# Performance work log

Hardware: AMD Instinct MI355X
Metric: run time of the kernel (lower is better)

Reference implementation:

```python
import jax, jax.numpy as jnp
import numpy as np

N_NODES = 50000
N_EDGES = 800000
HIDDEN = 128
N_GRAPHS = 32
EPS = 1e-5  # GraphNorm eps


def setup_inputs() -> dict:
    key = jax.random.key(0)
    ks = jax.random.split(key, 8)
    x = jax.random.normal(ks[0], (N_NODES, HIDDEN), dtype=jnp.float32)
    edge_index = jax.random.randint(ks[1], (2, N_EDGES), 0, N_NODES, dtype=jnp.int64)
    batch = jnp.sort(jax.random.randint(ks[2], (N_NODES,), 0, N_GRAPHS, dtype=jnp.int64))
    s = 1.0 / np.sqrt(HIDDEN)
    # SAGEConv: lin_l (applied to aggregated neighbors, with bias) and lin_r (root, no bias)
    W_l = jax.random.normal(ks[3], (HIDDEN, HIDDEN), dtype=jnp.float32) * s
    b_l = jnp.zeros((HIDDEN,), dtype=jnp.float32)
    W_r = jax.random.normal(ks[4], (HIDDEN, HIDDEN), dtype=jnp.float32) * s
    # GraphNorm params: weight, bias, mean_scale (alpha)
    gn_weight = jnp.ones((HIDDEN,), dtype=jnp.float32)
    gn_bias = jnp.zeros((HIDDEN,), dtype=jnp.float32)
    gn_mean_scale = jnp.ones((HIDDEN,), dtype=jnp.float32)
    return {
        "x": x, "edge_index": edge_index, "batch": batch,
        "W_l": W_l, "b_l": b_l, "W_r": W_r,
        "gn_weight": gn_weight, "gn_bias": gn_bias, "gn_mean_scale": gn_mean_scale,
    }


def reference(x, edge_index, batch, W_l, b_l, W_r, gn_weight, gn_bias, gn_mean_scale):
    src, dst = edge_index[0], edge_index[1]
    n = x.shape[0]
    # --- SAGEConv: mean aggregation of source features at destination ---
    msg_sum = jax.ops.segment_sum(x[src], dst, num_segments=n)          # [N, D]
    deg = jax.ops.segment_sum(jnp.ones((src.shape[0],), x.dtype), dst, num_segments=n)
    agg = msg_sum / jnp.maximum(deg, 1.0)[:, None]
    out = agg @ W_l + b_l + x @ W_r                                      # [N, D]
    # --- GraphNorm: per-graph mean/var with learnable mean scale alpha ---
    g_cnt = jax.ops.segment_sum(jnp.ones((n,), x.dtype), batch, num_segments=N_GRAPHS)[:, None]
    g_cnt = jnp.maximum(g_cnt, 1.0)
    mean = jax.ops.segment_sum(out, batch, num_segments=N_GRAPHS) / g_cnt  # [G, D]
    sub = out - gn_mean_scale * mean[batch]
    var = jax.ops.segment_sum(sub * sub, batch, num_segments=N_GRAPHS) / g_cnt
    normed = gn_weight * sub / jnp.sqrt(var[batch] + EPS) + gn_bias
    # --- exact GELU (torch nn.GELU default), dropout = identity (eval), residual ---
    return jax.nn.gelu(normed, approximate=False) + x
```

## Files before the change

kernel.cpp:

```cpp
#include <hip/hip_runtime.h>
#include <math.h>

#define NN 50000
#define NE 800000
#define HD 128
#define NG 32
#define GN_EPS 1e-5f
#define NSH 8

#define NBLK_R 800
#define CH_R   1000
#define NBUCK  196
#define NBB    (NBUCK * NBLK_R)
#define NCHS   ((NBB + 255) / 256)
#define DCAP   8192

typedef __bf16 v8bf __attribute__((ext_vector_type(8)));
typedef float f32x4 __attribute__((ext_vector_type(4)));

#define ROWPTR_OFF 0
#define BB_OFF     50016
#define CS_OFF     206816
#define GSUMS_OFF  207840
#define GSQS_OFF   240608
#define GCNTS_OFF  273376
#define MEAN_OFF   273632
#define RSTD_OFF   277728
#define SRCS_OFF   281824
#define PSRC_OFF   681824
#define PDLOW_OFF  1081824
#define WPACK_OFF  1281824
#define MEMSET_INTS (32768 + 32768 + 256)

__device__ __forceinline__ unsigned short f2bf(float f) {
  unsigned int u = __float_as_uint(f);
  u = (u + 0x7fffu + ((u >> 16) & 1u)) >> 16;
  return (unsigned short)u;
}
__device__ __forceinline__ float bf_lo(unsigned int u) { return __uint_as_float(u << 16); }
__device__ __forceinline__ float bf_hi(unsigned int u) { return __uint_as_float(u & 0xffff0000u); }

__global__ __launch_bounds__(256) void prep_k(const float* __restrict__ x,
    const float* __restrict__ Wl, const float* __restrict__ Wr,
    unsigned short* __restrict__ Abuf, unsigned short* __restrict__ wp,
    int* __restrict__ zbase) {
  int i = blockIdx.x * 256 + threadIdx.x;
  if (i < MEMSET_INTS) zbase[i] = 0;
  if (i < 32768) {
    int e = i & 7, lane = (i >> 3) & 63, nt = (i >> 9) & 7, ks = i >> 12;
    int k = ks * 32 + (lane >> 4) * 8 + e;
    int c = nt * 16 + (lane & 15);
    float v = (k < HD) ? Wl[k * HD + c] : Wr[(k - HD) * HD + c];
    wp[i] = f2bf(v);
  }
  if (i < NN * 16) {
    int n = i >> 4, seg = i & 15;
    const float* src = x + (size_t)n * HD + seg * 8;
    float4 v0 = *(const float4*)(src);
    float4 v1 = *(const float4*)(src + 4);
    uint4 o;
    o.x = (unsigned)f2bf(v0.x) | ((unsigned)f2bf(v0.y) << 16);
    o.y = (unsigned)f2bf(v0.z) | ((unsigned)f2bf(v0.w) << 16);
    o.z = (unsigned)f2bf(v1.x) | ((unsigned)f2bf(v1.y) << 16);
    o.w = (unsigned)f2bf(v1.z) | ((unsigned)f2bf(v1.w) << 16);
    *(uint4*)(Abuf + (size_t)n * 256 + 128 + seg * 8) = o;
  }
}


__global__ __launch_bounds__(256) void rhist_k(const int* __restrict__ ei,
                                               int* __restrict__ bb) {
  __shared__ int h[NBUCK];
  int tid = threadIdx.x, b = blockIdx.x;
  for (int i = tid; i < NBUCK; i += 256) h[i] = 0;
  __syncthreads();
  int base = b * CH_R;
  for (int j = tid; j < CH_R; j += 256)
    atomicAdd(&h[ei[NE + base + j] >> 8], 1);
  __syncthreads();
  for (int i = tid; i < NBUCK; i += 256) bb[i * NBLK_R + b] = h[i];
}

__global__ __launch_bounds__(256) void csum_k(const int* __restrict__ bb,
                                              int* __restrict__ cs) {
  __shared__ int red[4];
  int i = blockIdx.x * 256 + threadIdx.x;
  int v = (i < NBB) ? bb[i] : 0;
#pragma unroll
  for (int off = 32; off; off >>= 1) v += __shfl_down(v, off, 64);
  if ((threadIdx.x & 63) == 0) red[threadIdx.x >> 6] = v;
  __syncthreads();
  if (threadIdx.x == 0) cs[blockIdx.x] = red[0] + red[1] + red[2] + red[3];
}

__global__ __launch_bounds__(1024) void cscan_k(int* __restrict__ cs) {
  __shared__ int s[1024];
  int t = threadIdx.x;
  int v = (t < NCHS) ? cs[t] : 0;
  s[t] = v;
  __syncthreads();
  for (int off = 1; off < 1024; off <<= 1) {
    int u = (t >= off) ? s[t - off] : 0;
    __syncthreads();
    s[t] += u;
    __syncthreads();
  }
  if (t < NCHS) cs[t] = s[t] - v;
}

__global__ __launch_bounds__(256) void cfill_k(int* __restrict__ bb,
                                               const int* __restrict__ cs) {
  __shared__ int s[256];
  int t = threadIdx.x;
  int i = blockIdx.x * 256 + t;
  int c = (i < NBB) ? bb[i] : 0;
  s[t] = c;
  __syncthreads();
#pragma unroll
  for (int off = 1; off < 256; off <<= 1) {
    int u = (t >= off) ? s[t - off] : 0;
    __syncthreads();
    s[t] += u;
    __syncthreads();
  }
  if (i < NBB) bb[i] = cs[blockIdx.x] + s[t] - c;
}

__global__ __launch_bounds__(256) void rscatter_k(const int* __restrict__ ei,
    const int* __restrict__ bb, unsigned short* __restrict__ psrc,
    unsigned char* __restrict__ pdlow) {
  __shared__ int cur[NBUCK];
  int tid = threadIdx.x, b = blockIdx.x;
  for (int i = tid; i < NBUCK; i += 256) cur[i] = bb[i * NBLK_R + b];
  __syncthreads();
  int base = b * CH_R;
  for (int j = tid; j < CH_R; j += 256) {
    int e = base + j;
    int src = ei[e];
    int dst = ei[NE + e];
    int pos = atomicAdd(&cur[dst >> 8], 1);
    psrc[pos] = (unsigned short)src;
    pdlow[pos] = (unsigned char)(dst & 255);
  }
}

__global__ __launch_bounds__(256) void rfinal_k(const int* __restrict__ bb,
    const unsigned short* __restrict__ psrc, const unsigned char* __restrict__ pdlow,
    unsigned short* __restrict__ srcs, int* __restrict__ rowptr) {
  __shared__ unsigned short ssrc[DCAP];
  __shared__ unsigned short sout[DCAP];
  __shared__ unsigned char sdl[DCAP];
  __shared__ int h2[256], scn[256], cur2[256];
  int tid = threadIdx.x, k = blockIdx.x;
  int segB = bb[k * NBLK_R];
  int segE = (k == NBUCK - 1) ? NE : bb[(k + 1) * NBLK_R];
  int cnt = segE - segB;
  for (int j = tid; j < cnt; j += 256) {
    ssrc[j] = psrc[segB + j];
    sdl[j] = pdlow[segB + j];
  }
  h2[tid] = 0;
  __syncthreads();
  for (int j = tid; j < cnt; j += 256) atomicAdd(&h2[sdl[j]], 1);
  __syncthreads();
  scn[tid] = h2[tid];
  __syncthreads();
#pragma unroll
  for (int off = 1; off < 256; off <<= 1) {
    int u = (tid >= off) ? scn[tid - off] : 0;
    __syncthreads();
    scn[tid] += u;
    __syncthreads();
  }
  int excl = scn[tid] - h2[tid];
  cur2[tid] = excl;
  int dst = k * 256 + tid;
  if (dst < NN) rowptr[dst] = segB + excl;
  if (dst == NN - 1) rowptr[NN] = NE;
  __syncthreads();
  for (int j = tid; j < cnt; j += 256) {
    int p = atomicAdd(&cur2[sdl[j]], 1);
    sout[p] = ssrc[j];
  }
  __syncthreads();
  for (int j = tid; j < cnt; j += 256) srcs[segB + j] = sout[j];
}

__global__ __launch_bounds__(256) void gather_k(const int* __restrict__ rowptr,
    const unsigned short* __restrict__ srcs, unsigned short* Abuf) {
  int t = blockIdx.x * 256 + threadIdx.x;
  int n = t >> 4, q = t & 15;
  if (n >= NN) return;
  int b = rowptr[n], e = rowptr[n + 1];
  float a0=0,a1=0,a2=0,a3=0,a4=0,a5=0,a6=0,a7=0;
  int i = b;
  for (; i + 1 < e; i += 2) {
    int s0 = srcs[i], s1 = srcs[i + 1];
    uint4 v0 = *(const uint4*)(Abuf + (size_t)s0 * 256 + 128 + q * 8);
    uint4 v1 = *(const uint4*)(Abuf + (size_t)s1 * 256 + 128 + q * 8);
    a0 += bf_lo(v0.x) + bf_lo(v1.x);  a1 += bf_hi(v0.x) + bf_hi(v1.x);
    a2 += bf_lo(v0.y) + bf_lo(v1.y);  a3 += bf_hi(v0.y) + bf_hi(v1.y);
    a4 += bf_lo(v0.z) + bf_lo(v1.z);  a5 += bf_hi(v0.z) + bf_hi(v1.z);
    a6 += bf_lo(v0.w) + bf_lo(v1.w);  a7 += bf_hi(v0.w) + bf_hi(v1.w);
  }
  if (i < e) {
    int s0 = srcs[i];
    uint4 v0 = *(const uint4*)(Abuf + (size_t)s0 * 256 + 128 + q * 8);
    a0 += bf_lo(v0.x); a1 += bf_hi(v0.x);
    a2 += bf_lo(v0.y); a3 += bf_hi(v0.y);
    a4 += bf_lo(v0.z); a5 += bf_hi(v0.z);
    a6 += bf_lo(v0.w); a7 += bf_hi(v0.w);
  }
  float inv = 1.0f / fmaxf((float)(e - b), 1.0f);
  uint4 o;
  o.x = (unsigned)f2bf(a0 * inv) | ((unsigned)f2bf(a1 * inv) << 16);
  o.y = (unsigned)f2bf(a2 * inv) | ((unsigned)f2bf(a3 * inv) << 16);
  o.z = (unsigned)f2bf(a4 * inv) | ((unsigned)f2bf(a5 * inv) << 16);
  o.w = (unsigned)f2bf(a6 * inv) | ((unsigned)f2bf(a7 * inv) << 16);
  *(uint4*)(Abuf + (size_t)n * 256 + q * 8) = o;
}

__global__ __launch_bounds__(256) void gemm_k(const unsigned short* Abuf,
    const unsigned short* __restrict__ wp, const float* __restrict__ bl,
    const int* __restrict__ batch, float* out, float* __restrict__ gsumS,
    float* __restrict__ gsqS, float* __restrict__ gcntS) {
  __shared__ float lsum[16][136];
  __shared__ float lsq[16][136];
  __shared__ unsigned char ridx[64];
  __shared__ int sg0, snrun;
  int tid = threadIdx.x;
  int base0 = blockIdx.x * 64;
  int nvalid = min(64, NN - base0);
  if (tid == 0) {
    int g0 = batch[base0];
    sg0 = g0;
    snrun = batch[base0 + nvalid - 1] - g0 + 1;
  }
  __syncthreads();
  if (tid < 64)
    ridx[tid] = (tid < nvalid) ? (unsigned char)(batch[base0 + tid] - sg0)
                               : (unsigned char)0;
  __syncthreads();

  int shard = blockIdx.x & 7;
  float* gs = gsumS + shard * (NG * HD);
  float* gq = gsqS + shard * (NG * HD);
  float* gc = gcntS + shard * NG;

  int wave = tid >> 6;
  int lane = tid & 63;
  int base = base0 + wave * 16;
  int row = lane & 15, kg = lane >> 4;
  int node = base + row;
  if (node > NN - 1) node = NN - 1;
  const unsigned short* arow = Abuf + (size_t)node * 256 + kg * 8;
  f32x4 acc[8] = {};
#pragma unroll
  for (int ks = 0; ks < 8; ++ks) {
    v8bf a = __builtin_bit_cast(v8bf, *(const uint4*)(arow + ks * 32));
    const unsigned short* wrow = wp + ks * 4096 + lane * 8;
#pragma unroll
    for (int nt = 0; nt < 8; ++nt) {
      v8bf b = __builtin_bit_cast(v8bf, *(const uint4*)(wrow + nt * 512));
      acc[nt] = __builtin_amdgcn_mfma_f32_16x16x32_bf16(a, b, acc[nt], 0, 0, 0);
    }
  }
  int c0 = lane & 15;
  float bv[8];
#pragma unroll
  for (int nt = 0; nt < 8; ++nt) bv[nt] = bl[nt * 16 + c0];

  if (snrun == 1) {
    float ps0[8] = {}, pq0[8] = {};
#pragma unroll
    for (int j = 0; j < 4; ++j) {
      int n = base0 + wave * 16 + kg * 4 + j;
      if (n >= NN) break;
      float* orow = out + (size_t)n * HD;
#pragma unroll
      for (int nt = 0; nt < 8; ++nt) {
        float v = acc[nt][j] + bv[nt];
        orow[nt * 16 + c0] = v;
        ps0[nt] += v;
        pq0[nt] += v * v;
      }
    }
    int r = wave * 4 + kg;
#pragma unroll
    for (int nt = 0; nt < 8; ++nt) {
      lsum[r][nt * 16 + c0] = ps0[nt];
      lsq[r][nt * 16 + c0] = pq0[nt];
    }
    __syncthreads();
    if (tid < HD) {
      float s = 0.0f, q = 0.0f;
#pragma unroll
      for (int r2 = 0; r2 < 16; ++r2) { s += lsum[r2][tid]; q += lsq[r2][tid]; }
      atomicAdd(gs + sg0 * HD + tid, s);
      atomicAdd(gq + sg0 * HD + tid, q);
    }
    if (tid == 0) atomicAdd(gc + sg0, (float)nvalid);
  } else if (snrun == 2) {
    float ps0[8] = {}, pq0[8] = {}, ps1[8] = {}, pq1[8] = {};
#pragma unroll
    for (int j = 0; j < 4; ++j) {
      int rb = wave * 16 + kg * 4 + j;
      int n = base0 + rb;
      if (n >= NN) break;
      float* orow = out + (size_t)n * HD;
      bool b1 = (ridx[rb] != 0);
#pragma unroll
      for (int nt = 0; nt < 8; ++nt) {
        float v = acc[nt][j] + bv[nt];
        orow[nt * 16 + c0] = v;
        if (b1) { ps1[nt] += v; pq1[nt] += v * v; }
        else    { ps0[nt] += v; pq0[nt] += v * v; }
      }
    }
    int r = wave * 4 + kg;
#pragma unroll
    for (int nt = 0; nt < 8; ++nt) {
      lsum[r][nt * 16 + c0] = ps0[nt];
      lsq[r][nt * 16 + c0] = pq0[nt];
    }
    __syncthreads();
    if (tid < HD) {
      float s = 0.0f, q = 0.0f;
#pragma unroll
      for (int r2 = 0; r2 < 16; ++r2) { s += lsum[r2][tid]; q += lsq[r2][tid]; }
      atomicAdd(gs + sg0 * HD + tid, s);
      atomicAdd(gq + sg0 * HD + tid, q);
    }
    __syncthreads();
#pragma unroll
    for (int nt = 0; nt < 8; ++nt) {
      lsum[r][nt * 16 + c0] = ps1[nt];
      lsq[r][nt * 16 + c0] = pq1[nt];
    }
    __syncthreads();
    if (tid < HD) {
      float s = 0.0f, q = 0.0f;
#pragma unroll
      for (int r2 = 0; r2 < 16; ++r2) { s += lsum[r2][tid]; q += lsq[r2][tid]; }
      atomicAdd(gs + (sg0 + 1) * HD + tid, s);
      atomicAdd(gq + (sg0 + 1) * HD + tid, q);
    }
    if (tid == 0) {
      int n0 = 0;
      for (int r2 = 0; r2 < nvalid; ++r2) n0 += (ridx[r2] == 0);
      atomicAdd(gc + sg0, (float)n0);
      atomicAdd(gc + sg0 + 1, (float)(nvalid - n0));
    }
  } else {
#pragma unroll
    for (int j = 0; j < 4; ++j) {
      int rb = wave * 16 + kg * 4 + j;
      int n = base0 + rb;
      if (n >= NN) break;
      float* orow = out + (size_t)n * HD;
      int g = sg0 + ridx[rb];
#pragma unroll
      for (int nt = 0; nt < 8; ++nt) {
        float v = acc[nt][j] + bv[nt];
        orow[nt * 16 + c0] = v;
        atomicAdd(gs + g * HD + nt * 16 + c0, v);
        atomicAdd(gq + g * HD + nt * 16 + c0, v * v);
      }
    }
    if (tid < nvalid) atomicAdd(gc + batch[base0 + tid], 1.0f);
  }
}

__global__ __launch_bounds__(256) void finalize_k(const float* __restrict__ gsumS,
    const float* __restrict__ gsqS, const float* __restrict__ gcntS,
    const float* __restrict__ alpha, float* __restrict__ mean,
    float* __restrict__ rstd) {
  int i = blockIdx.x * 256 + threadIdx.x;
  if (i >= NG * HD) return;
  int g = i >> 7, d = i & 127;
  float s = 0.0f, q = 0.0f, cnt = 0.0f;
#pragma unroll
  for (int sh = 0; sh < NSH; ++sh) {
    s += gsumS[sh * (NG * HD) + i];
    q += gsqS[sh * (NG * HD) + i];
    cnt += gcntS[sh * NG + g];
  }
  cnt = fmaxf(cnt, 1.0f);
  float mu = s / cnt;
  float a = alpha[d];
  float var = q / cnt - mu * mu * (2.0f * a - a * a);
  mean[i] = mu;
  rstd[i] = rsqrtf(fmaxf(var, 0.0f) + GN_EPS);
}

__global__ __launch_bounds__(256) void final_k(float* __restrict__ out,
    const float* __restrict__ x, const int* __restrict__ batch,
    const float* __restrict__ mean, const float* __restrict__ rstd,
    const float* __restrict__ alpha, const float* __restrict__ gw,
    const float* __restrict__ gb) {
  size_t i = ((size_t)blockIdx.x * 256 + threadIdx.x) * 4;
  if (i >= (size_t)NN * HD) return;
  int n = (int)(i >> 7);
  int d = (int)(i & 127);
  int g = batch[n];
  float4 v  = *(float4*)(out + i);
  float4 xv = *(const float4*)(x + i);
  float4 al = *(const float4*)(alpha + d);
  float4 w  = *(const float4*)(gw + d);
  float4 b  = *(const float4*)(gb + d);
  float4 mn = *(const float4*)(mean + (size_t)g * HD + d);
  float4 rs = *(const float4*)(rstd + (size_t)g * HD + d);
  float vv[4] = {v.x, v.y, v.z, v.w};
  float xx[4] = {xv.x, xv.y, xv.z, xv.w};
  float aa[4] = {al.x, al.y, al.z, al.w};
  float ww[4] = {w.x, w.y, w.z, w.w};
  float bb2[4] = {b.x, b.y, b.z, b.w};
  float mm[4] = {mn.x, mn.y, mn.z, mn.w};
  float rr[4] = {rs.x, rs.y, rs.z, rs.w};
  float r[4];
#pragma unroll
  for (int c = 0; c < 4; ++c) {
    float sub = vv[c] - aa[c] * mm[c];
    float nm  = ww[c] * sub * rr[c] + bb2[c];
    float ge  = 0.5f * nm * (1.0f + erff(nm * 0.70710678118654752f));
    r[c] = ge + xx[c];
  }
  float4 res = {r[0], r[1], r[2], r[3]};
  *(float4*)(out + i) = res;
}

extern "C" void kernel_launch(void* const* d_in, const int* in_sizes, int n_in,
                              void* d_out, int out_size, void* d_ws, size_t ws_size,
                              hipStream_t stream) {
  const float* x     = (const float*)d_in[0];
  const int*   ei    = (const int*)d_in[1];
  const int*   batch = (const int*)d_in[2];
  const float* Wl    = (const float*)d_in[3];
  const float* bl    = (const float*)d_in[4];
  const float* Wr    = (const float*)d_in[5];
  const float* gw    = (const float*)d_in[6];
  const float* gb    = (const float*)d_in[7];
  const float* alpha = (const float*)d_in[8];

  float* out = (float*)d_out;
  unsigned short* Abuf = (unsigned short*)d_out;
  int*   wsi = (int*)d_ws;
  float* wsf = (float*)d_ws;
  int* rowptr = wsi + ROWPTR_OFF;
  int* bb     = wsi + BB_OFF;
  int* cs     = wsi + CS_OFF;
  float* gsumS = wsf + GSUMS_OFF;
  float* gsqS  = wsf + GSQS_OFF;
  float* gcntS = wsf + GCNTS_OFF;
  float* mean  = wsf + MEAN_OFF;
  float* rstd  = wsf + RSTD_OFF;
  unsigned short* srcs  = (unsigned short*)(wsi + SRCS_OFF);
  unsigned short* psrc  = (unsigned short*)(wsi + PSRC_OFF);
  unsigned char*  pdlow = (unsigned char*)(wsi + PDLOW_OFF);
  unsigned short* wpack = (unsigned short*)(wsi + WPACK_OFF);

  prep_k<<<3125, 256, 0, stream>>>(x, Wl, Wr, Abuf, wpack,
                                   (int*)(wsf + GSUMS_OFF));

  rhist_k<<<NBLK_R, 256, 0, stream>>>(ei, bb);
  csum_k<<<NCHS, 256, 0, stream>>>(bb, cs);
  cscan_k<<<1, 1024, 0, stream>>>(cs);
  cfill_k<<<NCHS, 256, 0, stream>>>(bb, cs);
  rscatter_k<<<NBLK_R, 256, 0, stream>>>(ei, bb, psrc, pdlow);
  rfinal_k<<<NBUCK, 256, 0, stream>>>(bb, psrc, pdlow, srcs, rowptr);

  gather_k<<<(NN * 16 + 255) / 256, 256, 0, stream>>>(rowptr, srcs, Abuf);

  gemm_k<<<(NN + 63) / 64, 256, 0, stream>>>(Abuf, wpack, bl, batch, out,
                                             gsumS, gsqS, gcntS);

  finalize_k<<<16, 256, 0, stream>>>(gsumS, gsqS, gcntS, alpha, mean, rstd);

  final_k<<<(NN * HD / 4 + 255) / 256, 256, 0, stream>>>(
      out, x, batch, mean, rstd, alpha, gw, gb);
}
```

Baseline: 106.1 us.

## Fuse neighbor gather into GEMM via LDS and merge prep with histogram

The mean-aggregation gather is moved into the GEMM kernel: each block computes the aggregated bf16 rows for its 64 nodes into shared memory and reads the root features from a separate compact bf16 buffer in the workspace. This removes one kernel launch and the global write and re-read of the aggregated half of the A buffer. The prep and destination-histogram kernels are merged into a single launch split by block index, and the histogram and scatter kernels now load edges as int4 vectors. The cost is extra LDS use and per-block gather latency ahead of the MFMA work, which may lower occupancy in the GEMM kernel.

```diff
diff --git a/kernel.cpp b/kernel.cpp
--- a/kernel.cpp
+++ b/kernel.cpp
@@ -14,6 +14,7 @@
 #define NBB    (NBUCK * NBLK_R)
 #define NCHS   ((NBB + 255) / 256)
 #define DCAP   8192
+#define PREP_BLKS 3125
 
 typedef __bf16 v8bf __attribute__((ext_vector_type(8)));
 typedef float f32x4 __attribute__((ext_vector_type(4)));
@@ -30,6 +31,7 @@
 #define PSRC_OFF   681824
 #define PDLOW_OFF  1081824
 #define WPACK_OFF  1281824
+#define ABX_OFF    1298208
 #define MEMSET_INTS (32768 + 32768 + 256)
 
 __device__ __forceinline__ unsigned short f2bf(float f) {
@@ -40,45 +42,49 @@
 __device__ __forceinline__ float bf_lo(unsigned int u) { return __uint_as_float(u << 16); }
 __device__ __forceinline__ float bf_hi(unsigned int u) { return __uint_as_float(u & 0xffff0000u); }
 
-__global__ __launch_bounds__(256) void prep_k(const float* __restrict__ x,
+__global__ __launch_bounds__(256) void prep_rhist_k(const float* __restrict__ x,
     const float* __restrict__ Wl, const float* __restrict__ Wr,
-    unsigned short* __restrict__ Abuf, unsigned short* __restrict__ wp,
-    int* __restrict__ zbase) {
-  int i = blockIdx.x * 256 + threadIdx.x;
-  if (i < MEMSET_INTS) zbase[i] = 0;
-  if (i < 32768) {
-    int e = i & 7, lane = (i >> 3) & 63, nt = (i >> 9) & 7, ks = i >> 12;
-    int k = ks * 32 + (lane >> 4) * 8 + e;
-    int c = nt * 16 + (lane & 15);
-    float v = (k < HD) ? Wl[k * HD + c] : Wr[(k - HD) * HD + c];
-    wp[i] = f2bf(v);
-  }
-  if (i < NN * 16) {
-    int n = i >> 4, seg = i & 15;
-    const float* src = x + (size_t)n * HD + seg * 8;
-    float4 v0 = *(const float4*)(src);
-    float4 v1 = *(const float4*)(src + 4);
-    uint4 o;
-    o.x = (unsigned)f2bf(v0.x) | ((unsigned)f2bf(v0.y) << 16);
-    o.y = (unsigned)f2bf(v0.z) | ((unsigned)f2bf(v0.w) << 16);
-    o.z = (unsigned)f2bf(v1.x) | ((unsigned)f2bf(v1.y) << 16);
-    o.w = (unsigned)f2bf(v1.z) | ((unsigned)f2bf(v1.w) << 16);
-    *(uint4*)(Abuf + (size_t)n * 256 + 128 + seg * 8) = o;
-  }
-}
-
-
-__global__ __launch_bounds__(256) void rhist_k(const int* __restrict__ ei,
-                                               int* __restrict__ bb) {
+    unsigned short* __restrict__ Abx, unsigned short* __restrict__ wp,
+    int* __restrict__ zbase, const int* __restrict__ ei, int* __restrict__ bb) {
   __shared__ int h[NBUCK];
-  int tid = threadIdx.x, b = blockIdx.x;
-  for (int i = tid; i < NBUCK; i += 256) h[i] = 0;
-  __syncthreads();
-  int base = b * CH_R;
-  for (int j = tid; j < CH_R; j += 256)
-    atomicAdd(&h[ei[NE + base + j] >> 8], 1);
-  __syncthreads();
-  for (int i = tid; i < NBUCK; i += 256) bb[i * NBLK_R + b] = h[i];
+  int tid = threadIdx.x;
+  if (blockIdx.x < PREP_BLKS) {
+    int i = blockIdx.x * 256 + tid;
+    if (i < MEMSET_INTS) zbase[i] = 0;
+    if (i < 32768) {
+      int e = i & 7, lane = (i >> 3) & 63, nt = (i >> 9) & 7, ks = i >> 12;
+      int k = ks * 32 + (lane >> 4) * 8 + e;
+      int c = nt * 16 + (lane & 15);
+      float v = (k < HD) ? Wl[k * HD + c] : Wr[(k - HD) * HD + c];
+      wp[i] = f2bf(v);
+    }
+    if (i < NN * 16) {
+      int n = i >> 4, seg = i & 15;
+      const float* src = x + (size_t)n * HD + seg * 8;
+      float4 v0 = *(const float4*)(src);
+      float4 v1 = *(const float4*)(src + 4);
+      uint4 o;
+      o.x = (unsigned)f2bf(v0.x) | ((unsigned)f2bf(v0.y) << 16);
+      o.y = (unsigned)f2bf(v0.z) | ((unsigned)f2bf(v0.w) << 16);
+      o.z = (unsigned)f2bf(v1.x) | ((unsigned)f2bf(v1.y) << 16);
+      o.w = (unsigned)f2bf(v1.z) | ((unsigned)f2bf(v1.w) << 16);
+      *(uint4*)(Abx + (size_t)n * HD + seg * 8) = o;
+    }
+  } else {
+    int b = blockIdx.x - PREP_BLKS;
+    for (int i = tid; i < NBUCK; i += 256) h[i] = 0;
+    __syncthreads();
+    int base = b * CH_R;
+    if (tid < CH_R / 4) {
+      int4 d = *(const int4*)(ei + NE + base + tid * 4);
+      atomicAdd(&h[d.x >> 8], 1);
+      atomicAdd(&h[d.y >> 8], 1);
+      atomicAdd(&h[d.z >> 8], 1);
+      atomicAdd(&h[d.w >> 8], 1);
+    }
+    __syncthreads();
+    for (int i = tid; i < NBUCK; i += 256) bb[i * NBLK_R + b] = h[i];
+  }
 }
 
 __global__ __launch_bounds__(256) void csum_k(const int* __restrict__ bb,
@@ -134,13 +140,14 @@
   for (int i = tid; i < NBUCK; i += 256) cur[i] = bb[i * NBLK_R + b];
   __syncthreads();
   int base = b * CH_R;
-  for (int j = tid; j < CH_R; j += 256) {
-    int e = base + j;
-    int src = ei[e];
-    int dst = ei[NE + e];
-    int pos = atomicAdd(&cur[dst >> 8], 1);
-    psrc[pos] = (unsigned short)src;
-    pdlow[pos] = (unsigned char)(dst & 255);
+  if (tid < CH_R / 4) {
+    int4 s4 = *(const int4*)(ei + base + tid * 4);
+    int4 d4 = *(const int4*)(ei + NE + base + tid * 4);
+    int p;
+    p = atomicAdd(&cur[d4.x >> 8], 1); psrc[p] = (unsigned short)s4.x; pdlow[p] = (unsigned char)(d4.x & 255);
+    p = atomicAdd(&cur[d4.y >> 8], 1); psrc[p] = (unsigned short)s4.y; pdlow[p] = (unsigned char)(d4.y & 255);
+    p = atomicAdd(&cur[d4.z >> 8], 1); psrc[p] = (unsigned short)s4.z; pdlow[p] = (unsigned char)(d4.z & 255);
+    p = atomicAdd(&cur[d4.w >> 8], 1); psrc[p] = (unsigned short)s4.w; pdlow[p] = (unsigned char)(d4.w & 255);
   }
 }
 
@@ -186,44 +193,13 @@
   for (int j = tid; j < cnt; j += 256) srcs[segB + j] = sout[j];
 }
 
-__global__ __launch_bounds__(256) void gather_k(const int* __restrict__ rowptr,
-    const unsigned short* __restrict__ srcs, unsigned short* Abuf) {
-  int t = blockIdx.x * 256 + threadIdx.x;
-  int n = t >> 4, q = t & 15;
-  if (n >= NN) return;
-  int b = rowptr[n], e = rowptr[n + 1];
-  float a0=0,a1=0,a2=0,a3=0,a4=0,a5=0,a6=0,a7=0;
-  int i = b;
-  for (; i + 1 < e; i += 2) {
-    int s0 = srcs[i], s1 = srcs[i + 1];
-    uint4 v0 = *(const uint4*)(Abuf + (size_t)s0 * 256 + 128 + q * 8);
-    uint4 v1 = *(const uint4*)(Abuf + (size_t)s1 * 256 + 128 + q * 8);
-    a0 += bf_lo(v0.x) + bf_lo(v1.x);  a1 += bf_hi(v0.x) + bf_hi(v1.x);
-    a2 += bf_lo(v0.y) + bf_lo(v1.y);  a3 += bf_hi(v0.y) + bf_hi(v1.y);
-    a4 += bf_lo(v0.z) + bf_lo(v1.z);  a5 += bf_hi(v0.z) + bf_hi(v1.z);
-    a6 += bf_lo(v0.w) + bf_lo(v1.w);  a7 += bf_hi(v0.w) + bf_hi(v1.w);
-  }
-  if (i < e) {
-    int s0 = srcs[i];
-    uint4 v0 = *(const uint4*)(Abuf + (size_t)s0 * 256 + 128 + q * 8);
-    a0 += bf_lo(v0.x); a1 += bf_hi(v0.x);
-    a2 += bf_lo(v0.y); a3 += bf_hi(v0.y);
-    a4 += bf_lo(v0.z); a5 += bf_hi(v0.z);
-    a6 += bf_lo(v0.w); a7 += bf_hi(v0.w);
-  }
-  float inv = 1.0f / fmaxf((float)(e - b), 1.0f);
-  uint4 o;
-  o.x = (unsigned)f2bf(a0 * inv) | ((unsigned)f2bf(a1 * inv) << 16);
-  o.y = (unsigned)f2bf(a2 * inv) | ((unsigned)f2bf(a3 * inv) << 16);
-  o.z = (unsigned)f2bf(a4 * inv) | ((unsigned)f2bf(a5 * inv) << 16);
-  o.w = (unsigned)f2bf(a6 * inv) | ((unsigned)f2bf(a7 * inv) << 16);
-  *(uint4*)(Abuf + (size_t)n * 256 + q * 8) = o;
-}
-
-__global__ __launch_bounds__(256) void gemm_k(const unsigned short* Abuf,
+__global__ __launch_bounds__(256) void gemm_k(const unsigned short* __restrict__ Abx,
+    const int* __restrict__ rowptr, const unsigned short* __restrict__ srcs,
     const unsigned short* __restrict__ wp, const float* __restrict__ bl,
-    const int* __restrict__ batch, float* out, float* __restrict__ gsumS,
-    float* __restrict__ gsqS, float* __restrict__ gcntS) {
+    const int* __restrict__ batch, float* __restrict__ out,
+    float* __restrict__ gsumS, float* __restrict__ gsqS,
+    float* __restrict__ gcntS) {
+  __shared__ unsigned short agg[64][136];
   __shared__ float lsum[16][136];
   __shared__ float lsq[16][136];
   __shared__ unsigned char ridx[64];
@@ -236,10 +212,46 @@
     sg0 = g0;
     snrun = batch[base0 + nvalid - 1] - g0 + 1;
   }
-  __syncthreads();
-  if (tid < 64)
-    ridx[tid] = (tid < nvalid) ? (unsigned char)(batch[base0 + tid] - sg0)
+  if (tid < 64) {
+    int nb = base0 + tid;
+    ridx[tid] = (tid < nvalid) ? (unsigned char)(batch[nb] - batch[base0])
                                : (unsigned char)0;
+  }
+
+#pragma unroll
+  for (int pass = 0; pass < 4; ++pass) {
+    int nl = pass * 16 + (tid >> 4);
+    int q = tid & 15;
+    int n = base0 + nl;
+    if (n > NN - 1) n = NN - 1;
+    int b = rowptr[n], e = rowptr[n + 1];
+    float a0=0,a1=0,a2=0,a3=0,a4=0,a5=0,a6=0,a7=0;
+    int i = b;
+    for (; i + 1 < e; i += 2) {
+      int s0 = srcs[i], s1 = srcs[i + 1];
+      uint4 v0 = *(const uint4*)(Abx + (size_t)s0 * HD + q * 8);
+      uint4 v1 = *(const uint4*)(Abx + (size_t)s1 * HD + q * 8);
+      a0 += bf_lo(v0.x) + bf_lo(v1.x);  a1 += bf_hi(v0.x) + bf_hi(v1.x);
+      a2 += bf_lo(v0.y) + bf_lo(v1.y);  a3 += bf_hi(v0.y) + bf_hi(v1.y);
+      a4 += bf_lo(v0.z) + bf_lo(v1.z);  a5 += bf_hi(v0.z) + bf_hi(v1.z);
+      a6 += bf_lo(v0.w) + bf_lo(v1.w);  a7 += bf_hi(v0.w) + bf_hi(v1.w);
+    }
+    if (i < e) {
+      int s0 = srcs[i];
+      uint4 v0 = *(const uint4*)(Abx + (size_t)s0 * HD + q * 8);
+      a0 += bf_lo(v0.x); a1 += bf_hi(v0.x);
+      a2 += bf_lo(v0.y); a3 += bf_hi(v0.y);
+      a4 += bf_lo(v0.z); a5 += bf_hi(v0.z);
+      a6 += bf_lo(v0.w); a7 += bf_hi(v0.w);
+    }
+    float inv = 1.0f / fmaxf((float)(e - b), 1.0f);
+    uint4 o;
+    o.x = (unsigned)f2bf(a0 * inv) | ((unsigned)f2bf(a1 * inv) << 16);
+    o.y = (unsigned)f2bf(a2 * inv) | ((unsigned)f2bf(a3 * inv) << 16);
+    o.z = (unsigned)f2bf(a4 * inv) | ((unsigned)f2bf(a5 * inv) << 16);
+    o.w = (unsigned)f2bf(a6 * inv) | ((unsigned)f2bf(a7 * inv) << 16);
+    *(uint4*)(&agg[nl][q * 8]) = o;
+  }
   __syncthreads();
 
   int shard = blockIdx.x & 7;
@@ -249,15 +261,17 @@
 
   int wave = tid >> 6;
   int lane = tid & 63;
-  int base = base0 + wave * 16;
   int row = lane & 15, kg = lane >> 4;
-  int node = base + row;
+  int arow_l = wave * 16 + row;
+  int node = base0 + arow_l;
   if (node > NN - 1) node = NN - 1;
-  const unsigned short* arow = Abuf + (size_t)node * 256 + kg * 8;
   f32x4 acc[8] = {};
 #pragma unroll
   for (int ks = 0; ks < 8; ++ks) {
-    v8bf a = __builtin_bit_cast(v8bf, *(const uint4*)(arow + ks * 32));
+    const unsigned short* aptr = (ks < 4)
+        ? &agg[arow_l][ks * 32 + kg * 8]
+        : Abx + (size_t)node * HD + (ks - 4) * 32 + kg * 8;
+    v8bf a = __builtin_bit_cast(v8bf, *(const uint4*)aptr);
     const unsigned short* wrow = wp + ks * 4096 + lane * 8;
 #pragma unroll
     for (int nt = 0; nt < 8; ++nt) {
@@ -443,7 +457,6 @@
   const float* alpha = (const float*)d_in[8];
 
   float* out = (float*)d_out;
-  unsigned short* Abuf = (unsigned short*)d_out;
   int*   wsi = (int*)d_ws;
   float* wsf = (float*)d_ws;
   int* rowptr = wsi + ROWPTR_OFF;
@@ -458,21 +471,19 @@
   unsigned short* psrc  = (unsigned short*)(wsi + PSRC_OFF);
   unsigned char*  pdlow = (unsigned char*)(wsi + PDLOW_OFF);
   unsigned short* wpack = (unsigned short*)(wsi + WPACK_OFF);
-
-  prep_k<<<3125, 256, 0, stream>>>(x, Wl, Wr, Abuf, wpack,
-                                   (int*)(wsf + GSUMS_OFF));
-
-  rhist_k<<<NBLK_R, 256, 0, stream>>>(ei, bb);
+  unsigned short* Abx   = (unsigned short*)(wsi + ABX_OFF);
+
+  prep_rhist_k<<<PREP_BLKS + NBLK_R, 256, 0, stream>>>(
+      x, Wl, Wr, Abx, wpack, (int*)(wsf + GSUMS_OFF), ei, bb);
+
   csum_k<<<NCHS, 256, 0, stream>>>(bb, cs);
   cscan_k<<<1, 1024, 0, stream>>>(cs);
   cfill_k<<<NCHS, 256, 0, stream>>>(bb, cs);
   rscatter_k<<<NBLK_R, 256, 0, stream>>>(ei, bb, psrc, pdlow);
   rfinal_k<<<NBUCK, 256, 0, stream>>>(bb, psrc, pdlow, srcs, rowptr);
 
-  gather_k<<<(NN * 16 + 255) / 256, 256, 0, stream>>>(rowptr, srcs, Abuf);
-
-  gemm_k<<<(NN + 63) / 64, 256, 0, stream>>>(Abuf, wpack, bl, batch, out,
-                                             gsumS, gsqS, gcntS);
+  gemm_k<<<(NN + 63) / 64, 256, 0, stream>>>(Abx, rowptr, srcs, wpack, bl,
+                                             batch, out, gsumS, gsqS, gcntS);
 
   finalize_k<<<16, 256, 0, stream>>>(gsumS, gsqS, gcntS, alpha, mean, rstd);
 
```

New measurement: 107.2 us. No clear change (+1.0%).

## Fuse prep and histogram kernels, vectorize edge loads, move Abuf to workspace

Applied to the files above, without the earlier changes.

Merges the bf16 conversion/weight-pack kernel and the radix histogram kernel into one launch, with the extra blocks doing the histogram, removing one launch and letting the two overlap. The histogram and scatter kernels now read edge indices as int4, handling four edges per thread. Abuf moves from the output buffer into the workspace, and gemm_k gets __restrict__ on its pointers, which allows more aggressive load scheduling. The cost is a larger workspace footprint, and it assumes the workspace is big enough for Abuf.

```diff
diff --git a/kernel.cpp b/kernel.cpp
--- a/kernel.cpp
+++ b/kernel.cpp
@@ -14,6 +14,7 @@
 #define NBB    (NBUCK * NBLK_R)
 #define NCHS   ((NBB + 255) / 256)
 #define DCAP   8192
+#define PREP_BLKS 3125
 
 typedef __bf16 v8bf __attribute__((ext_vector_type(8)));
 typedef float f32x4 __attribute__((ext_vector_type(4)));
@@ -30,6 +31,7 @@
 #define PSRC_OFF   681824
 #define PDLOW_OFF  1081824
 #define WPACK_OFF  1281824
+#define ABUF_OFF   1298208
 #define MEMSET_INTS (32768 + 32768 + 256)
 
 __device__ __forceinline__ unsigned short f2bf(float f) {
@@ -40,45 +42,49 @@
 __device__ __forceinline__ float bf_lo(unsigned int u) { return __uint_as_float(u << 16); }
 __device__ __forceinline__ float bf_hi(unsigned int u) { return __uint_as_float(u & 0xffff0000u); }
 
-__global__ __launch_bounds__(256) void prep_k(const float* __restrict__ x,
+__global__ __launch_bounds__(256) void prep_rhist_k(const float* __restrict__ x,
     const float* __restrict__ Wl, const float* __restrict__ Wr,
     unsigned short* __restrict__ Abuf, unsigned short* __restrict__ wp,
-    int* __restrict__ zbase) {
-  int i = blockIdx.x * 256 + threadIdx.x;
-  if (i < MEMSET_INTS) zbase[i] = 0;
-  if (i < 32768) {
-    int e = i & 7, lane = (i >> 3) & 63, nt = (i >> 9) & 7, ks = i >> 12;
-    int k = ks * 32 + (lane >> 4) * 8 + e;
-    int c = nt * 16 + (lane & 15);
-    float v = (k < HD) ? Wl[k * HD + c] : Wr[(k - HD) * HD + c];
-    wp[i] = f2bf(v);
-  }
-  if (i < NN * 16) {
-    int n = i >> 4, seg = i & 15;
-    const float* src = x + (size_t)n * HD + seg * 8;
-    float4 v0 = *(const float4*)(src);
-    float4 v1 = *(const float4*)(src + 4);
-    uint4 o;
-    o.x = (unsigned)f2bf(v0.x) | ((unsigned)f2bf(v0.y) << 16);
-    o.y = (unsigned)f2bf(v0.z) | ((unsigned)f2bf(v0.w) << 16);
-    o.z = (unsigned)f2bf(v1.x) | ((unsigned)f2bf(v1.y) << 16);
-    o.w = (unsigned)f2bf(v1.z) | ((unsigned)f2bf(v1.w) << 16);
-    *(uint4*)(Abuf + (size_t)n * 256 + 128 + seg * 8) = o;
-  }
-}
-
-
-__global__ __launch_bounds__(256) void rhist_k(const int* __restrict__ ei,
-                                               int* __restrict__ bb) {
+    int* __restrict__ zbase, const int* __restrict__ ei, int* __restrict__ bb) {
   __shared__ int h[NBUCK];
-  int tid = threadIdx.x, b = blockIdx.x;
-  for (int i = tid; i < NBUCK; i += 256) h[i] = 0;
-  __syncthreads();
-  int base = b * CH_R;
-  for (int j = tid; j < CH_R; j += 256)
-    atomicAdd(&h[ei[NE + base + j] >> 8], 1);
-  __syncthreads();
-  for (int i = tid; i < NBUCK; i += 256) bb[i * NBLK_R + b] = h[i];
+  int tid = threadIdx.x;
+  if (blockIdx.x < PREP_BLKS) {
+    int i = blockIdx.x * 256 + tid;
+    if (i < MEMSET_INTS) zbase[i] = 0;
+    if (i < 32768) {
+      int e = i & 7, lane = (i >> 3) & 63, nt = (i >> 9) & 7, ks = i >> 12;
+      int k = ks * 32 + (lane >> 4) * 8 + e;
+      int c = nt * 16 + (lane & 15);
+      float v = (k < HD) ? Wl[k * HD + c] : Wr[(k - HD) * HD + c];
+      wp[i] = f2bf(v);
+    }
+    if (i < NN * 16) {
+      int n = i >> 4, seg = i & 15;
+      const float* src = x + (size_t)n * HD + seg * 8;
+      float4 v0 = *(const float4*)(src);
+      float4 v1 = *(const float4*)(src + 4);
+      uint4 o;
+      o.x = (unsigned)f2bf(v0.x) | ((unsigned)f2bf(v0.y) << 16);
+      o.y = (unsigned)f2bf(v0.z) | ((unsigned)f2bf(v0.w) << 16);
+      o.z = (unsigned)f2bf(v1.x) | ((unsigned)f2bf(v1.y) << 16);
+      o.w = (unsigned)f2bf(v1.z) | ((unsigned)f2bf(v1.w) << 16);
+      *(uint4*)(Abuf + (size_t)n * 256 + 128 + seg * 8) = o;
+    }
+  } else {
+    int b = blockIdx.x - PREP_BLKS;
+    for (int i = tid; i < NBUCK; i += 256) h[i] = 0;
+    __syncthreads();
+    int base = b * CH_R;
+    if (tid < CH_R / 4) {
+      int4 d = *(const int4*)(ei + NE + base + tid * 4);
+      atomicAdd(&h[d.x >> 8], 1);
+      atomicAdd(&h[d.y >> 8], 1);
+      atomicAdd(&h[d.z >> 8], 1);
+      atomicAdd(&h[d.w >> 8], 1);
+    }
+    __syncthreads();
+    for (int i = tid; i < NBUCK; i += 256) bb[i * NBLK_R + b] = h[i];
+  }
 }
 
 __global__ __launch_bounds__(256) void csum_k(const int* __restrict__ bb,
@@ -134,13 +140,14 @@
   for (int i = tid; i < NBUCK; i += 256) cur[i] = bb[i * NBLK_R + b];
   __syncthreads();
   int base = b * CH_R;
-  for (int j = tid; j < CH_R; j += 256) {
-    int e = base + j;
-    int src = ei[e];
-    int dst = ei[NE + e];
-    int pos = atomicAdd(&cur[dst >> 8], 1);
-    psrc[pos] = (unsigned short)src;
-    pdlow[pos] = (unsigned char)(dst & 255);
+  if (tid < CH_R / 4) {
+    int4 s4 = *(const int4*)(ei + base + tid * 4);
+    int4 d4 = *(const int4*)(ei + NE + base + tid * 4);
+    int p;
+    p = atomicAdd(&cur[d4.x >> 8], 1); psrc[p] = (unsigned short)s4.x; pdlow[p] = (unsigned char)(d4.x & 255);
+    p = atomicAdd(&cur[d4.y >> 8], 1); psrc[p] = (unsigned short)s4.y; pdlow[p] = (unsigned char)(d4.y & 255);
+    p = atomicAdd(&cur[d4.z >> 8], 1); psrc[p] = (unsigned short)s4.z; pdlow[p] = (unsigned char)(d4.z & 255);
+    p = atomicAdd(&cur[d4.w >> 8], 1); psrc[p] = (unsigned short)s4.w; pdlow[p] = (unsigned char)(d4.w & 255);
   }
 }
 
@@ -220,10 +227,11 @@
   *(uint4*)(Abuf + (size_t)n * 256 + q * 8) = o;
 }
 
-__global__ __launch_bounds__(256) void gemm_k(const unsigned short* Abuf,
+__global__ __launch_bounds__(256) void gemm_k(const unsigned short* __restrict__ Abuf,
     const unsigned short* __restrict__ wp, const float* __restrict__ bl,
-    const int* __restrict__ batch, float* out, float* __restrict__ gsumS,
-    float* __restrict__ gsqS, float* __restrict__ gcntS) {
+    const int* __restrict__ batch, float* __restrict__ out,
+    float* __restrict__ gsumS, float* __restrict__ gsqS,
+    float* __restrict__ gcntS) {
   __shared__ float lsum[16][136];
   __shared__ float lsq[16][136];
   __shared__ unsigned char ridx[64];
@@ -443,7 +451,6 @@
   const float* alpha = (const float*)d_in[8];
 
   float* out = (float*)d_out;
-  unsigned short* Abuf = (unsigned short*)d_out;
   int*   wsi = (int*)d_ws;
   float* wsf = (float*)d_ws;
   int* rowptr = wsi + ROWPTR_OFF;
@@ -458,11 +465,11 @@
   unsigned short* psrc  = (unsigned short*)(wsi + PSRC_OFF);
   unsigned char*  pdlow = (unsigned char*)(wsi + PDLOW_OFF);
   unsigned short* wpack = (unsigned short*)(wsi + WPACK_OFF);
-
-  prep_k<<<3125, 256, 0, stream>>>(x, Wl, Wr, Abuf, wpack,
-                                   (int*)(wsf + GSUMS_OFF));
-
-  rhist_k<<<NBLK_R, 256, 0, stream>>>(ei, bb);
+  unsigned short* Abuf  = (unsigned short*)(wsi + ABUF_OFF);
+
+  prep_rhist_k<<<PREP_BLKS + NBLK_R, 256, 0, stream>>>(
+      x, Wl, Wr, Abuf, wpack, (int*)(wsf + GSUMS_OFF), ei, bb);
+
   csum_k<<<NCHS, 256, 0, stream>>>(bb, cs);
   cscan_k<<<1, 1024, 0, stream>>>(cs);
   cfill_k<<<NCHS, 256, 0, stream>>>(bb, cs);
```

Result: faster. 103.2 us (-2.8%).
